# Optimization experiments

Hardware: AMD Instinct MI355X
Metric: run time of the kernel (lower is better)

The kernel has to match this reference:

```python
import jax, jax.numpy as jnp
import numpy as np

B, H, W, C, NH, WS, SS = 16, 112, 112, 384, 12, 7, 3
HD = C // NH          # head dim = 32
N = WS * WS           # tokens per window = 49
MLP_H = 4 * C         # 1536
NW = (H // WS) * (W // WS)  # windows per image = 256


def _rel_pos_index():
    coords = np.stack(np.meshgrid(np.arange(WS), np.arange(WS), indexing='ij')).reshape(2, -1)
    rel = (coords[:, :, None] - coords[:, None, :]).transpose(1, 2, 0)  # (N, N, 2)
    rel[..., 0] += WS - 1
    rel[..., 1] += WS - 1
    rel[..., 0] *= 2 * WS - 1
    return rel.sum(-1)  # (N, N) in [0, (2WS-1)^2)


def _attn_mask():
    img = np.zeros((H, W))
    cnt = 0
    slices = (slice(0, -WS), slice(-WS, -SS), slice(-SS, None))
    for hs in slices:
        for ws_ in slices:
            img[hs, ws_] = cnt
            cnt += 1
    mw = img.reshape(H // WS, WS, W // WS, WS).transpose(0, 2, 1, 3).reshape(-1, N)
    am = mw[:, None, :] - mw[:, :, None]
    return np.where(am != 0, -100.0, 0.0).astype(np.float32)  # (NW, N, N)


REL_IDX = jnp.asarray(_rel_pos_index().reshape(-1))  # (N*N,) int
MASK = jnp.asarray(_attn_mask())                      # (NW, N, N)


def _ln(x, g, b, eps=1e-5):
    m = jnp.mean(x, -1, keepdims=True)
    v = jnp.mean((x - m) ** 2, -1, keepdims=True)
    return (x - m) / jnp.sqrt(v + eps) * g + b


def setup_inputs() -> dict:
    key = jax.random.key(0)
    ks = jax.random.split(key, 16)
    s = 0.02
    return {
        'x': jax.random.normal(ks[0], (B, H * W, C), jnp.float32),
        'norm1_g': jnp.ones((C,), jnp.float32),
        'norm1_b': jnp.zeros((C,), jnp.float32),
        'qkv_w': jax.random.normal(ks[1], (C, 3 * C), jnp.float32) * s,
        'qkv_b': jnp.zeros((3 * C,), jnp.float32),
        'proj_w': jax.random.normal(ks[2], (C, C), jnp.float32) * s,
        'proj_b': jnp.zeros((C,), jnp.float32),
        'rpb_table': jax.random.normal(ks[3], ((2 * WS - 1) ** 2, NH), jnp.float32) * s,
        'norm2_g': jnp.ones((C,), jnp.float32),
        'norm2_b': jnp.zeros((C,), jnp.float32),
        'fc1_w': jax.random.normal(ks[4], (C, MLP_H), jnp.float32) * s,
        'fc1_b': jnp.zeros((MLP_H,), jnp.float32),
        'fc2_w': jax.random.normal(ks[5], (MLP_H, C), jnp.float32) * s,
        'fc2_b': jnp.zeros((C,), jnp.float32),
    }


def reference(x, norm1_g, norm1_b, qkv_w, qkv_b, proj_w, proj_b, rpb_table,
              norm2_g, norm2_b, fc1_w, fc1_b, fc2_w, fc2_b):
    shortcut = x
    h = _ln(x, norm1_g, norm1_b).reshape(B, H, W, C)
    # cyclic shift
    h = jnp.roll(h, (-SS, -SS), axis=(1, 2))
    # window partition -> (B*NW, N, C)
    wins = h.reshape(B, H // WS, WS, W // WS, WS, C).transpose(0, 1, 3, 2, 4, 5).reshape(-1, N, C)
    qkv = (wins @ qkv_w + qkv_b).reshape(-1, N, 3, NH, HD).transpose(2, 0, 3, 1, 4)
    q, k, v = qkv[0] * HD ** -0.5, qkv[1], qkv[2]  # (B*NW, NH, N, HD)
    attn = jnp.einsum('bhnd,bhmd->bhnm', q, k)
    bias = rpb_table[REL_IDX].reshape(N, N, NH).transpose(2, 0, 1)  # (NH, N, N)
    attn = attn + bias[None]
    attn = (attn.reshape(B, NW, NH, N, N) + MASK[None, :, None]).reshape(-1, NH, N, N)
    attn = jax.nn.softmax(attn, axis=-1)
    out = jnp.einsum('bhnm,bhmd->bhnd', attn, v).transpose(0, 2, 1, 3).reshape(-1, N, C)
    out = out @ proj_w + proj_b
    # window reverse
    out = out.reshape(B, H // WS, W // WS, WS, WS, C).transpose(0, 1, 3, 2, 4, 5).reshape(B, H, W, C)
    out = jnp.roll(out, (SS, SS), axis=(1, 2)).reshape(B, H * W, C)
    x = shortcut + out
    h2 = _ln(x, norm2_g, norm2_b)
    h2 = jax.nn.gelu(h2 @ fc1_w + fc1_b, approximate=False) @ fc2_w + fc2_b
    return x + h2
```

## Files before the change

### kernel.cpp

```cpp
#include <hip/hip_runtime.h>
#include <hip/hip_bf16.h>

typedef short bf16x8 __attribute__((ext_vector_type(8)));
typedef float f32x4 __attribute__((ext_vector_type(4)));
typedef float f32x16 __attribute__((ext_vector_type(16)));
typedef unsigned int u32x4 __attribute__((ext_vector_type(4)));

typedef __attribute__((address_space(1))) void gvoid;
typedef __attribute__((address_space(3))) void lvoid;

__device__ __forceinline__ short f2b(float f) {
  __hip_bfloat16 h = __float2bfloat16(f);
  return __builtin_bit_cast(short, h);
}

__device__ __forceinline__ f32x4 mfma16(bf16x8 a, bf16x8 b, f32x4 c) {
  return __builtin_amdgcn_mfma_f32_16x16x32_bf16(a, b, c, 0, 0, 0);
}

__device__ __forceinline__ f32x16 mfma32(bf16x8 a, bf16x8 b, f32x16 c) {
  return __builtin_amdgcn_mfma_f32_32x32x16_bf16(a, b, c, 0, 0, 0);
}

__device__ __forceinline__ unsigned cvtpk(float lo, float hi) {
  unsigned r;
  asm("v_cvt_pk_bf16_f32 %0, %1, %2" : "=v"(r) : "v"(lo), "v"(hi));
  return r;
}

__device__ __forceinline__ void gload16(const void* g, void* l) {
  __builtin_amdgcn_global_load_lds((const gvoid*)g, (lvoid*)l, 16, 0, 0);
}

__global__ __launch_bounds__(256) void convT_k(const float* __restrict__ src,
                                               short* __restrict__ dst, int K,
                                               int N, int scale_cols,
                                               float scale) {
  int idx = blockIdx.x * 256 + threadIdx.x;
  if (idx >= N * K) return;
  int n = idx / K, k = idx % K;
  float v = src[(size_t)k * N + n];
  if (n < scale_cols) v *= scale;
  dst[idx] = f2b(v);
}

__global__ __launch_bounds__(256) void scale_bias_k(const float* __restrict__ src,
                                                    float* __restrict__ dst,
                                                    int n, int scale_cols,
                                                    float scale) {
  int i = blockIdx.x * 256 + threadIdx.x;
  if (i >= n) return;
  dst[i] = src[i] * (i < scale_cols ? scale : 1.f);
}

__global__ __launch_bounds__(256) void biasmask_k(const float* __restrict__ rpb,
                                                  float* __restrict__ tbl) {
  int idx = blockIdx.x * 256 + threadIdx.x;
  int q = idx & 63, key = (idx >> 6) & 63;
  int hc = idx >> 12;
  int h = hc % 12, cls = hc / 12;
  float v;
  if (q >= 49 || key >= 49) {
    v = -1e4f;
  } else {
    int i1 = q / 7, j1 = q % 7, i2 = key / 7, j2 = key % 7;
    v = rpb[(size_t)((i1 - i2 + 6) * 13 + (j1 - j2 + 6)) * 12 + h];
    int clsh = cls >> 1, clsw = cls & 1;
    int rq = (clsh ? 1 + (i1 >= 4) : 0) * 3 + (clsw ? 1 + (j1 >= 4) : 0);
    int rk = (clsh ? 1 + (i2 >= 4) : 0) * 3 + (clsw ? 1 + (j2 >= 4) : 0);
    if (rq != rk) v -= 100.f;
  }
  tbl[idx] = v;
}

template <bool GATHER>
__device__ __forceinline__ void ln_body(const float* __restrict__ x,
                                        const float* __restrict__ gw,
                                        const float* __restrict__ bw,
                                        short* __restrict__ out) {
  const int lane = threadIdx.x & 63;
  const int t = (blockIdx.x << 2) + (threadIdx.x >> 6);
  size_t srow;
  if (GATHER) {
    int bb = t / 12544, rm2 = t % 12544;
    int wi = rm2 / 49, nn = rm2 % 49;
    int wh = wi >> 4, ww = wi & 15;
    int ii = nn / 7, jj = nn % 7;
    int rr = wh * 7 + ii + 3; if (rr >= 112) rr -= 112;
    int cc = ww * 7 + jj + 3; if (cc >= 112) cc -= 112;
    srow = ((size_t)bb * 12544 + rr * 112 + cc) * 384;
  } else {
    srow = (size_t)t * 384;
  }
  const float2* src = (const float2*)(x + srow);
  const float2* g2 = (const float2*)gw;
  const float2* b2 = (const float2*)bw;
  float2 u[3];
  float s = 0.f, ss = 0.f;
#pragma unroll
  for (int k = 0; k < 3; ++k) {
    u[k] = src[lane + (k << 6)];
    s += u[k].x + u[k].y;
    ss += u[k].x * u[k].x + u[k].y * u[k].y;
  }
#pragma unroll
  for (int m = 1; m < 64; m <<= 1) {
    s += __shfl_xor(s, m, 64);
    ss += __shfl_xor(ss, m, 64);
  }
  const float mean = s * (1.f / 384.f);
  const float var = ss * (1.f / 384.f) - mean * mean;
  const float rstd = rsqrtf(var + 1e-5f);
  unsigned* o = (unsigned*)(out + (size_t)t * 384);
#pragma unroll
  for (int k = 0; k < 3; ++k) {
    int c = lane + (k << 6);
    float2 gv = g2[c], bv = b2[c];
    unsigned lo = (unsigned short)f2b((u[k].x - mean) * rstd * gv.x + bv.x);
    unsigned hi = (unsigned short)f2b((u[k].y - mean) * rstd * gv.y + bv.y);
    o[c] = lo | (hi << 16);
  }
}

__global__ __launch_bounds__(256) void ln1_k(const float* __restrict__ x,
                                             const float* __restrict__ gw,
                                             const float* __restrict__ bw,
                                             short* __restrict__ out) {
  ln_body<true>(x, gw, bw, out);
}
__global__ __launch_bounds__(256) void ln2_k(const float* __restrict__ x,
                                             const float* __restrict__ gw,
                                             const float* __restrict__ bw,
                                             short* __restrict__ out) {
  ln_body<false>(x, gw, bw, out);
}

template <int EPI>
__device__ __forceinline__ void gemm_body(
    const short* __restrict__ A, int lda, const short* __restrict__ BT,
    int ldb, const float* __restrict__ bias, int K, short* __restrict__ outh,
    int ldo, float* __restrict__ outf, const float* __restrict__ resid) {
  __shared__ __align__(16) short As0[4096], Bs0[4096];
  __shared__ __align__(16) short As1[4096], Bs1[4096];
  const int tid = threadIdx.x;
  const int gx = gridDim.x;
  int lin = blockIdx.y * gx + blockIdx.x;
  const int cpx = (gx * gridDim.y) >> 3;
  lin = (lin & 7) * cpx + (lin >> 3);
  const int m0 = (lin / gx) << 7, n0 = (lin % gx) << 7;
  const int lane = tid & 63;
  const int wave = tid >> 6;
  const int wr = (wave >> 1) << 6, wc = (wave & 1) << 6;
  const int g = lane >> 4, q = lane & 15;
  const int loff = tid << 3;

  f32x4 acc[4][4];
#pragma unroll
  for (int i = 0; i < 4; ++i)
#pragma unroll
    for (int j = 0; j < 4; ++j) acc[i][j] = (f32x4){0.f, 0.f, 0.f, 0.f};

  const short* Ab = A + (size_t)(m0 + (tid >> 2)) * lda + ((tid & 3) << 3);
  const short* Ab2 = Ab + (size_t)64 * lda;
  const short* Bb = BT + (size_t)(n0 + (tid >> 2)) * ldb + ((tid & 3) << 3);
  const short* Bb2 = Bb + (size_t)64 * ldb;

#define STAGE(kt, dA, dB)                   \
  do {                                      \
    gload16(Ab + (kt), &dA[loff]);          \
    gload16(Ab2 + (kt), &dA[loff + 2048]);  \
    gload16(Bb + (kt), &dB[loff]);          \
    gload16(Bb2 + (kt), &dB[loff + 2048]);  \
  } while (0)

#define COMPUTE(SA, SB)                                               \
  do {                                                                \
    bf16x8 af[4], bfv[4];                                             \
    _Pragma("unroll") for (int mi = 0; mi < 4; ++mi)                  \
        af[mi] = *(const bf16x8*)&SA[(wr + mi * 16 + q) * 32 + g * 8];\
    _Pragma("unroll") for (int ni = 0; ni < 4; ++ni)                  \
        bfv[ni] = *(const bf16x8*)&SB[(wc + ni * 16 + q) * 32 + g * 8];\
    _Pragma("unroll") for (int mi = 0; mi < 4; ++mi)                  \
        _Pragma("unroll") for (int ni = 0; ni < 4; ++ni)              \
            acc[mi][ni] = mfma16(af[mi], bfv[ni], acc[mi][ni]);       \
  } while (0)

  const int nt = K >> 5;
  STAGE(0, As0, Bs0);
  __syncthreads();
  for (int t = 0; t < nt; t += 2) {
    STAGE((t + 1) << 5, As1, Bs1);
    COMPUTE(As0, Bs0);
    __syncthreads();
    if (t + 2 < nt) STAGE((t + 2) << 5, As0, Bs0);
    COMPUTE(As1, Bs1);
    __syncthreads();
  }
#undef STAGE
#undef COMPUTE

  float bv[4];
#pragma unroll
  for (int ni = 0; ni < 4; ++ni)
    bv[ni] = bias ? bias[n0 + wc + ni * 16 + q] : 0.f;

#pragma unroll
  for (int mi = 0; mi < 4; ++mi) {
#pragma unroll
    for (int r = 0; r < 4; ++r) {
      const int grow = m0 + wr + mi * 16 + g * 4 + r;
      size_t orow;
      if constexpr (EPI == 2) {
        int bb = grow / 12544, rm2 = grow % 12544;
        int wi = rm2 / 49, nn = rm2 % 49;
        int wh = wi >> 4, ww = wi & 15;
        int ii = nn / 7, jj = nn % 7;
        int rr = wh * 7 + ii + 3; if (rr >= 112) rr -= 112;
        int cc = ww * 7 + jj + 3; if (cc >= 112) cc -= 112;
        orow = ((size_t)bb * 12544 + rr * 112 + cc) * 384;
      } else {
        orow = (size_t)grow * (size_t)ldo;
      }
#pragma unroll
      for (int ni = 0; ni < 4; ++ni) {
        const int gcol = n0 + wc + ni * 16 + q;
        float v = acc[mi][ni][r] + bv[ni];
        if constexpr (EPI == 0) {
          outh[orow + gcol] = f2b(v);
        } else if constexpr (EPI == 1) {
          v = 0.5f * v * (1.f + erff(v * 0.70710678118f));
          outh[orow + gcol] = f2b(v);
        } else if constexpr (EPI == 2) {
          outf[orow + gcol] = resid[orow + gcol] + v;
        } else {
          outf[orow + gcol] += v;
        }
      }
    }
  }
}

#define GEMM_WRAP(NAME, EPI)                                                   \
  __global__ __launch_bounds__(256) void NAME(                                 \
      const short* __restrict__ A, int lda, const short* __restrict__ BT,      \
      int ldb, const float* __restrict__ bias, int K,                          \
      short* __restrict__ outh, int ldo, float* __restrict__ outf,             \
      const float* __restrict__ resid) {                                       \
    gemm_body<EPI>(A, lda, BT, ldb, bias, K, outh, ldo, outf, resid);          \
  }
GEMM_WRAP(gemm_qkv_k, 0)
GEMM_WRAP(gemm_fc1_k, 1)
GEMM_WRAP(gemm_proj_k, 2)
GEMM_WRAP(gemm_fc2_k, 3)

__global__ __launch_bounds__(256) void attn_k(const short* __restrict__ qkv,
                                              const float* __restrict__ tbl,
                                              short* __restrict__ out) {
  const int lane = threadIdx.x & 63;
  const int task = blockIdx.x * 4 + (threadIdx.x >> 6);
  const int win = task / 12;
  const int h = task - win * 12;
  const int wh = (win >> 4) & 15, ww = win & 15;
  const int cls = ((wh == 15) ? 2 : 0) + ((ww == 15) ? 1 : 0);
  const int l31 = lane & 31, h5 = lane >> 5;
  const size_t tokbase = (size_t)win * 49;
  const short* base = qkv + tokbase * 1152 + h * 32;
  const bf16x8 zero8 = {0, 0, 0, 0, 0, 0, 0, 0};

  bf16x8 kf[2][2];
#pragma unroll
  for (int mi = 0; mi < 2; ++mi) {
    int row = l31 + 32 * mi;
#pragma unroll
    for (int s = 0; s < 2; ++s)
      kf[mi][s] = (row < 49)
                      ? *(const bf16x8*)(base + (size_t)row * 1152 + 384 +
                                         16 * s + 8 * h5)
                      : zero8;
  }
  bf16x8 vf[4];
#pragma unroll
  for (int kt = 0; kt < 4; ++kt) {
#pragma unroll
    for (int e = 0; e < 8; ++e) {
      int key = 16 * kt + 8 * h5 + e;
      vf[kt][e] = (key < 49) ? base[(size_t)key * 1152 + 768 + l31] : (short)0;
    }
  }

  const float* tb = tbl + ((size_t)(cls * 12 + h) << 12);

#pragma unroll
  for (int ni = 0; ni < 2; ++ni) {
    bf16x8 qf[2];
    int qrow = l31 + 32 * ni;
#pragma unroll
    for (int s = 0; s < 2; ++s)
      qf[s] = (qrow < 49)
                  ? *(const bf16x8*)(base + (size_t)qrow * 1152 + 16 * s +
                                     8 * h5)
                  : zero8;
    f32x16 st[2];
#pragma unroll
    for (int mi = 0; mi < 2; ++mi) {
      st[mi] = mfma32(kf[mi][0], qf[0], (f32x16)(0.f));
      st[mi] = mfma32(kf[mi][1], qf[1], st[mi]);
    }
#pragma unroll
    for (int mi = 0; mi < 2; ++mi)
#pragma unroll
      for (int r = 0; r < 16; ++r) {
        int koff = (r & 3) + 8 * (r >> 2) + 4 * h5;
        st[mi][r] += tb[(size_t)(32 * mi + koff) * 64 + 32 * ni + l31];
      }
    float mx = st[0][0];
#pragma unroll
    for (int r = 1; r < 16; ++r) mx = fmaxf(mx, st[0][r]);
#pragma unroll
    for (int r = 0; r < 16; ++r) mx = fmaxf(mx, st[1][r]);
    mx = fmaxf(mx, __shfl_xor(mx, 32, 64));
    float sm = 0.f;
#pragma unroll
    for (int mi = 0; mi < 2; ++mi)
#pragma unroll
      for (int r = 0; r < 16; ++r) {
        float e = __expf(st[mi][r] - mx);
        st[mi][r] = e;
        sm += e;
      }
    sm += __shfl_xor(sm, 32, 64);
    const float rinv = 1.f / sm;
#pragma unroll
    for (int mi = 0; mi < 2; ++mi)
#pragma unroll
      for (int r = 0; r < 16; ++r) st[mi][r] *= rinv;

    f32x16 acc = (f32x16)(0.f);
#pragma unroll
    for (int kt = 0; kt < 4; ++kt) {
      const int mi = kt >> 1, b8 = (kt & 1) * 8;
      unsigned q0l = cvtpk(st[mi][b8 + 0], st[mi][b8 + 1]);
      unsigned q0h = cvtpk(st[mi][b8 + 2], st[mi][b8 + 3]);
      unsigned q1l = cvtpk(st[mi][b8 + 4], st[mi][b8 + 5]);
      unsigned q1h = cvtpk(st[mi][b8 + 6], st[mi][b8 + 7]);
      unsigned sl = h5 ? q0l : q1l, sh = h5 ? q0h : q1h;
      unsigned kl = h5 ? q1l : q0l, kh = h5 ? q1h : q0h;
      unsigned rl = (unsigned)__shfl_xor((int)sl, 32, 64);
      unsigned rh = (unsigned)__shfl_xor((int)sh, 32, 64);
      u32x4 fr;
      fr[0] = h5 ? rl : kl;
      fr[1] = h5 ? rh : kh;
      fr[2] = h5 ? kl : rl;
      fr[3] = h5 ? kh : rh;
      acc = mfma32(__builtin_bit_cast(bf16x8, fr), vf[kt], acc);
    }
#pragma unroll
    for (int r = 0; r < 16; ++r) {
      int query = 32 * ni + (r & 3) + 8 * (r >> 2) + 4 * h5;
      if (ni == 0 || query < 49)
        out[(tokbase + query) * 384 + h * 32 + l31] = f2b(acc[r]);
    }
  }
}

extern "C" void kernel_launch(void* const* d_in, const int* in_sizes, int n_in,
                              void* d_out, int out_size, void* d_ws,
                              size_t ws_size, hipStream_t stream) {
  const float* x = (const float*)d_in[0];
  const float* n1g = (const float*)d_in[1];
  const float* n1b = (const float*)d_in[2];
  const float* qkvw = (const float*)d_in[3];
  const float* qkvb = (const float*)d_in[4];
  const float* projw = (const float*)d_in[5];
  const float* projb = (const float*)d_in[6];
  const float* rpb = (const float*)d_in[7];
  const float* n2g = (const float*)d_in[8];
  const float* n2b = (const float*)d_in[9];
  const float* fc1w = (const float*)d_in[10];
  const float* fc1b = (const float*)d_in[11];
  const float* fc2w = (const float*)d_in[12];
  const float* fc2b = (const float*)d_in[13];
  float* out = (float*)d_out;

  char* ws = (char*)d_ws;
  short* w_qkvT = (short*)(ws + 0);
  short* w_projT = (short*)(ws + 884736);
  short* w_fc1T = (short*)(ws + 1179648);
  short* w_fc2T = (short*)(ws + 2359296);
  float* w_qb = (float*)(ws + 3538944);
  float* tbl = (float*)(ws + 3543552);
  const size_t o_qkv = 4329984;
  short* qkvbuf = (short*)(ws + o_qkv);
  const size_t o_hwin = o_qkv + 462422016ull;
  short* hwin = (short*)(ws + o_hwin);
  const size_t o_fc1 = o_hwin + 154140672ull;

  int NC;
  size_t fc1_off = o_fc1;
  if (ws_size >= o_fc1 + 616562688ull) NC = 1;
  else if (ws_size >= o_fc1 + 308281344ull) NC = 2;
  else if (ws_size >= o_fc1 + 154140672ull) NC = 4;
  else { NC = 4; fc1_off = o_hwin; }
  short* fc1c = (short*)(ws + fc1_off);
  short* h2 = qkvbuf;

  const float qscale = 0.17677669529663687f;

  convT_k<<<(442368 + 255) / 256, 256, 0, stream>>>(qkvw, w_qkvT, 384, 1152, 384, qscale);
  convT_k<<<(147456 + 255) / 256, 256, 0, stream>>>(projw, w_projT, 384, 384, 0, 1.f);
  convT_k<<<(589824 + 255) / 256, 256, 0, stream>>>(fc1w, w_fc1T, 384, 1536, 0, 1.f);
  convT_k<<<(589824 + 255) / 256, 256, 0, stream>>>(fc2w, w_fc2T, 1536, 384, 0, 1.f);
  scale_bias_k<<<5, 256, 0, stream>>>(qkvb, w_qb, 1152, 384, qscale);
  biasmask_k<<<768, 256, 0, stream>>>(rpb, tbl);

  ln1_k<<<50176, 256, 0, stream>>>(x, n1g, n1b, hwin);
  gemm_qkv_k<<<dim3(9, 1568), 256, 0, stream>>>(hwin, 384, w_qkvT, 384, w_qb,
                                                384, qkvbuf, 1152, nullptr,
                                                nullptr);
  attn_k<<<12288, 256, 0, stream>>>(qkvbuf, tbl, hwin);
  gemm_proj_k<<<dim3(3, 1568), 256, 0, stream>>>(hwin, 384, w_projT, 384,
                                                 projb, 384, nullptr, 384, out,
                                                 x);
  ln2_k<<<50176, 256, 0, stream>>>(out, n2g, n2b, h2);
  const int CK = 1536 / NC;
  for (int c = 0; c < NC; ++c) {
    gemm_fc1_k<<<dim3(CK >> 7, 1568), 256, 0, stream>>>(
        h2, 384, w_fc1T + (size_t)c * CK * 384, 384, fc1b + c * CK, 384, fc1c,
        CK, nullptr, nullptr);
    gemm_fc2_k<<<dim3(3, 1568), 256, 0, stream>>>(
        fc1c, CK, w_fc2T + c * CK, 1536, (c == 0) ? fc2b : nullptr, CK,
        nullptr, 384, out, nullptr);
  }
}
```

Baseline: 2.159 ms.

## Triple-buffer GEMM LDS pipeline with partial vmcnt waits and MFMA priority

Converts the GEMM main loop from double-buffered LDS staging with full __syncthreads to a three-stage ring. Two tiles are kept in flight, and s_waitcnt vmcnt(4) plus a raw barrier wait only for the oldest tile. It also raises wave priority around the MFMA block and adds a launch-bounds occupancy hint of 3 blocks per CU. The aim is to hide global-load latency behind compute. In exchange, LDS use grows from 32KB to 48KB per block, which can limit occupancy, and the hand-written waitcnt logic depends on the exact count of outstanding loads.

```diff
diff --git a/kernel.cpp b/kernel.cpp
--- a/kernel.cpp
+++ b/kernel.cpp
@@ -140,8 +140,9 @@
     const short* __restrict__ A, int lda, const short* __restrict__ BT,
     int ldb, const float* __restrict__ bias, int K, short* __restrict__ outh,
     int ldo, float* __restrict__ outf, const float* __restrict__ resid) {
-  __shared__ __align__(16) short As0[4096], Bs0[4096];
-  __shared__ __align__(16) short As1[4096], Bs1[4096];
+  __shared__ __align__(16) short A0[4096], B0[4096];
+  __shared__ __align__(16) short A1[4096], B1[4096];
+  __shared__ __align__(16) short A2[4096], B2[4096];
   const int tid = threadIdx.x;
   const int gx = gridDim.x;
   int lin = blockIdx.y * gx + blockIdx.x;
@@ -180,24 +181,43 @@
         af[mi] = *(const bf16x8*)&SA[(wr + mi * 16 + q) * 32 + g * 8];\
     _Pragma("unroll") for (int ni = 0; ni < 4; ++ni)                  \
         bfv[ni] = *(const bf16x8*)&SB[(wc + ni * 16 + q) * 32 + g * 8];\
+    __builtin_amdgcn_s_setprio(1);                                    \
     _Pragma("unroll") for (int mi = 0; mi < 4; ++mi)                  \
         _Pragma("unroll") for (int ni = 0; ni < 4; ++ni)              \
             acc[mi][ni] = mfma16(af[mi], bfv[ni], acc[mi][ni]);       \
+    __builtin_amdgcn_s_setprio(0);                                    \
   } while (0)
 
+#define VM4 asm volatile("s_waitcnt vmcnt(4)" ::: "memory")
+#define VM0 asm volatile("s_waitcnt vmcnt(0)" ::: "memory")
+#define BAR __builtin_amdgcn_s_barrier()
+
   const int nt = K >> 5;
-  STAGE(0, As0, Bs0);
-  __syncthreads();
-  for (int t = 0; t < nt; t += 2) {
-    STAGE((t + 1) << 5, As1, Bs1);
-    COMPUTE(As0, Bs0);
-    __syncthreads();
-    if (t + 2 < nt) STAGE((t + 2) << 5, As0, Bs0);
-    COMPUTE(As1, Bs1);
-    __syncthreads();
+  STAGE(0, A0, B0);
+  STAGE(32, A1, B1);
+  VM4;
+  BAR;
+  for (int t = 0; t < nt; t += 3) {
+    if (t + 2 < nt) STAGE((t + 2) << 5, A2, B2);
+    COMPUTE(A0, B0);
+    if (t + 2 < nt) VM4; else VM0;
+    BAR;
+    if (t + 1 >= nt) break;
+    if (t + 3 < nt) STAGE((t + 3) << 5, A0, B0);
+    COMPUTE(A1, B1);
+    if (t + 3 < nt) VM4; else VM0;
+    BAR;
+    if (t + 2 >= nt) break;
+    if (t + 4 < nt) STAGE((t + 4) << 5, A1, B1);
+    COMPUTE(A2, B2);
+    if (t + 4 < nt) VM4; else VM0;
+    BAR;
   }
 #undef STAGE
 #undef COMPUTE
+#undef VM4
+#undef VM0
+#undef BAR
 
   float bv[4];
 #pragma unroll
@@ -241,7 +261,7 @@
 }
 
 #define GEMM_WRAP(NAME, EPI)                                                   \
-  __global__ __launch_bounds__(256) void NAME(                                 \
+  __global__ __launch_bounds__(256, 3) void NAME(                              \
       const short* __restrict__ A, int lda, const short* __restrict__ BT,      \
       int ldb, const float* __restrict__ bias, int K,                          \
       short* __restrict__ outh, int ldo, float* __restrict__ outf,             \
```

Measured after the change: 6.819 ms. 216% more time.

## Stream GEMM B operand via registers and triple-buffer swizzled A tiles

Applied to the files above, without the earlier changes.

The GEMM main loop is restructured. The B (weight) fragments are now loaded straight from global memory into registers, one k-step ahead, instead of being staged through LDS. A tiles are triple-buffered in LDS with an XOR swizzle that is meant to avoid bank conflicts. Explicit vmcnt waits and raw s_barrier replace __syncthreads, so the global loads for the next two k-steps can overlap the MFMA work. The aim is to cut LDS traffic and barrier stalls, at the cost of less coalesced B loads that rely on L2 hits, and a hand-unrolled loop whose tail is only correct for particular values of K/32.

```diff
diff --git a/kernel.cpp b/kernel.cpp
--- a/kernel.cpp
+++ b/kernel.cpp
@@ -140,8 +140,9 @@
     const short* __restrict__ A, int lda, const short* __restrict__ BT,
     int ldb, const float* __restrict__ bias, int K, short* __restrict__ outh,
     int ldo, float* __restrict__ outf, const float* __restrict__ resid) {
-  __shared__ __align__(16) short As0[4096], Bs0[4096];
-  __shared__ __align__(16) short As1[4096], Bs1[4096];
+  __shared__ __align__(16) short A0s[4096];
+  __shared__ __align__(16) short A1s[4096];
+  __shared__ __align__(16) short A2s[4096];
   const int tid = threadIdx.x;
   const int gx = gridDim.x;
   int lin = blockIdx.y * gx + blockIdx.x;
@@ -153,6 +154,8 @@
   const int wr = (wave >> 1) << 6, wc = (wave & 1) << 6;
   const int g = lane >> 4, q = lane & 15;
   const int loff = tid << 3;
+  const int cswz = (tid & 3) ^ ((tid >> 3) & 3);
+  const int cpos = (g ^ ((q >> 1) & 3)) << 3;
 
   f32x4 acc[4][4];
 #pragma unroll
@@ -160,44 +163,88 @@
 #pragma unroll
     for (int j = 0; j < 4; ++j) acc[i][j] = (f32x4){0.f, 0.f, 0.f, 0.f};
 
-  const short* Ab = A + (size_t)(m0 + (tid >> 2)) * lda + ((tid & 3) << 3);
+  const short* Ab = A + (size_t)(m0 + (tid >> 2)) * lda + cswz * 8;
   const short* Ab2 = Ab + (size_t)64 * lda;
-  const short* Bb = BT + (size_t)(n0 + (tid >> 2)) * ldb + ((tid & 3) << 3);
-  const short* Bb2 = Bb + (size_t)64 * ldb;
-
-#define STAGE(kt, dA, dB)                   \
-  do {                                      \
-    gload16(Ab + (kt), &dA[loff]);          \
-    gload16(Ab2 + (kt), &dA[loff + 2048]);  \
-    gload16(Bb + (kt), &dB[loff]);          \
-    gload16(Bb2 + (kt), &dB[loff + 2048]);  \
-  } while (0)
-
-#define COMPUTE(SA, SB)                                               \
-  do {                                                                \
-    bf16x8 af[4], bfv[4];                                             \
-    _Pragma("unroll") for (int mi = 0; mi < 4; ++mi)                  \
-        af[mi] = *(const bf16x8*)&SA[(wr + mi * 16 + q) * 32 + g * 8];\
-    _Pragma("unroll") for (int ni = 0; ni < 4; ++ni)                  \
-        bfv[ni] = *(const bf16x8*)&SB[(wc + ni * 16 + q) * 32 + g * 8];\
-    _Pragma("unroll") for (int mi = 0; mi < 4; ++mi)                  \
-        _Pragma("unroll") for (int ni = 0; ni < 4; ++ni)              \
-            acc[mi][ni] = mfma16(af[mi], bfv[ni], acc[mi][ni]);       \
-  } while (0)
-
+  const short* Bq = BT + (size_t)(n0 + wc + q) * ldb + g * 8;
+  const size_t bstep = (size_t)16 * ldb;
+
+#define STAGE_A(kt, DA)                    \
+  do {                                     \
+    gload16(Ab + (kt), &DA[loff]);         \
+    gload16(Ab2 + (kt), &DA[loff + 2048]); \
+  } while (0)
+
+#define BLOAD(BF, kt)                                                     \
+  do {                                                                    \
+    _Pragma("unroll") for (int ni = 0; ni < 4; ++ni)                      \
+        BF[ni] = *(const bf16x8*)(Bq + (size_t)ni * bstep + (kt));        \
+  } while (0)
+
+#define COMPUTE(SA, BF)                                                   \
+  do {                                                                    \
+    bf16x8 af[4];                                                         \
+    _Pragma("unroll") for (int mi = 0; mi < 4; ++mi)                      \
+        af[mi] = *(const bf16x8*)&SA[(wr + mi * 16 + q) * 32 + cpos];     \
+    _Pragma("unroll") for (int mi = 0; mi < 4; ++mi)                      \
+        _Pragma("unroll") for (int ni = 0; ni < 4; ++ni)                  \
+            acc[mi][ni] = mfma16(af[mi], BF[ni], acc[mi][ni]);            \
+  } while (0)
+
+#define VMW2                                          \
+  do {                                                \
+    asm volatile("s_waitcnt vmcnt(2)" ::: "memory");  \
+    __builtin_amdgcn_sched_barrier(0);                \
+  } while (0)
+#define VMW0                                          \
+  do {                                                \
+    asm volatile("s_waitcnt vmcnt(0)" ::: "memory");  \
+    __builtin_amdgcn_sched_barrier(0);                \
+  } while (0)
+#define BAR __builtin_amdgcn_s_barrier()
+
+  bf16x8 bfA[4], bfB[4];
   const int nt = K >> 5;
-  STAGE(0, As0, Bs0);
-  __syncthreads();
-  for (int t = 0; t < nt; t += 2) {
-    STAGE((t + 1) << 5, As1, Bs1);
-    COMPUTE(As0, Bs0);
-    __syncthreads();
-    if (t + 2 < nt) STAGE((t + 2) << 5, As0, Bs0);
-    COMPUTE(As1, Bs1);
-    __syncthreads();
-  }
-#undef STAGE
+
+  BLOAD(bfA, 0);
+  STAGE_A(0, A0s);
+  STAGE_A(32, A1s);
+  VMW2;
+  BAR;
+
+#define PH(BFC, BFN, SCUR, SNXT, tt)     \
+  do {                                   \
+    BLOAD(BFN, ((tt) + 1) << 5);         \
+    STAGE_A(((tt) + 2) << 5, SNXT);      \
+    COMPUTE(SCUR, BFC);                  \
+    VMW2;                                \
+    BAR;                                 \
+  } while (0)
+
+  int t = 0;
+  for (; t + 6 < nt; t += 6) {
+    PH(bfA, bfB, A0s, A2s, t + 0);
+    PH(bfB, bfA, A1s, A0s, t + 1);
+    PH(bfA, bfB, A2s, A1s, t + 2);
+    PH(bfB, bfA, A0s, A2s, t + 3);
+    PH(bfA, bfB, A1s, A0s, t + 4);
+    PH(bfB, bfA, A2s, A1s, t + 5);
+  }
+  PH(bfA, bfB, A0s, A2s, t + 0);
+  PH(bfB, bfA, A1s, A0s, t + 1);
+  PH(bfA, bfB, A2s, A1s, t + 2);
+  PH(bfB, bfA, A0s, A2s, t + 3);
+  BLOAD(bfB, (t + 5) << 5);
+  COMPUTE(A1s, bfA);
+  VMW0;
+  BAR;
+  COMPUTE(A2s, bfB);
+#undef STAGE_A
+#undef BLOAD
 #undef COMPUTE
+#undef VMW2
+#undef VMW0
+#undef BAR
+#undef PH
 
   float bv[4];
 #pragma unroll
```

New measurement: 2.709 ms. +25.5%, slower.

## Double GEMM K-tile to 64 and XOR-swizzle LDS layout

Applied to the files above, without the earlier changes.

The GEMM body now stages 64-wide K tiles instead of 32, which halves the number of barriers and pipeline iterations per block. Global loads write into LDS using an XOR-swizzled column order, and the MFMA fragment reads apply the matching swizzle to avoid LDS bank conflicts. LDS use per block doubles to 64 KB, which may lower occupancy. K must now be a multiple of 128 for the two-buffer loop to stay correct.

```diff
diff --git a/kernel.cpp b/kernel.cpp
--- a/kernel.cpp
+++ b/kernel.cpp
@@ -140,8 +140,8 @@
     const short* __restrict__ A, int lda, const short* __restrict__ BT,
     int ldb, const float* __restrict__ bias, int K, short* __restrict__ outh,
     int ldo, float* __restrict__ outf, const float* __restrict__ resid) {
-  __shared__ __align__(16) short As0[4096], Bs0[4096];
-  __shared__ __align__(16) short As1[4096], Bs1[4096];
+  __shared__ __align__(16) short A0s[8192], B0s[8192];
+  __shared__ __align__(16) short A1s[8192], B1s[8192];
   const int tid = threadIdx.x;
   const int gx = gridDim.x;
   int lin = blockIdx.y * gx + blockIdx.x;
@@ -152,7 +152,11 @@
   const int wave = tid >> 6;
   const int wr = (wave >> 1) << 6, wc = (wave & 1) << 6;
   const int g = lane >> 4, q = lane & 15;
-  const int loff = tid << 3;
+  const int q7 = q & 7;
+  const int rd0 = ((g) ^ q7) << 3;
+  const int rd1 = ((4 + g) ^ q7) << 3;
+  const int cswz = ((tid & 7) ^ ((tid >> 3) & 7)) << 3;
+  const int ldst = tid << 3;
 
   f32x4 acc[4][4];
 #pragma unroll
@@ -160,40 +164,41 @@
 #pragma unroll
     for (int j = 0; j < 4; ++j) acc[i][j] = (f32x4){0.f, 0.f, 0.f, 0.f};
 
-  const short* Ab = A + (size_t)(m0 + (tid >> 2)) * lda + ((tid & 3) << 3);
-  const short* Ab2 = Ab + (size_t)64 * lda;
-  const short* Bb = BT + (size_t)(n0 + (tid >> 2)) * ldb + ((tid & 3) << 3);
-  const short* Bb2 = Bb + (size_t)64 * ldb;
-
-#define STAGE(kt, dA, dB)                   \
-  do {                                      \
-    gload16(Ab + (kt), &dA[loff]);          \
-    gload16(Ab2 + (kt), &dA[loff + 2048]);  \
-    gload16(Bb + (kt), &dB[loff]);          \
-    gload16(Bb2 + (kt), &dB[loff + 2048]);  \
+  const short* Abase = A + (size_t)(m0 + (tid >> 3)) * lda + cswz;
+  const short* Bbase = BT + (size_t)(n0 + (tid >> 3)) * ldb + cswz;
+
+#define STAGE(kt, DA, DB)                                                     \
+  do {                                                                        \
+    _Pragma("unroll") for (int p = 0; p < 4; ++p) {                           \
+      gload16(Abase + (size_t)(32 * p) * lda + (kt), &DA[2048 * p + ldst]);   \
+      gload16(Bbase + (size_t)(32 * p) * ldb + (kt), &DB[2048 * p + ldst]);   \
+    }                                                                         \
   } while (0)
 
-#define COMPUTE(SA, SB)                                               \
-  do {                                                                \
-    bf16x8 af[4], bfv[4];                                             \
-    _Pragma("unroll") for (int mi = 0; mi < 4; ++mi)                  \
-        af[mi] = *(const bf16x8*)&SA[(wr + mi * 16 + q) * 32 + g * 8];\
-    _Pragma("unroll") for (int ni = 0; ni < 4; ++ni)                  \
-        bfv[ni] = *(const bf16x8*)&SB[(wc + ni * 16 + q) * 32 + g * 8];\
-    _Pragma("unroll") for (int mi = 0; mi < 4; ++mi)                  \
-        _Pragma("unroll") for (int ni = 0; ni < 4; ++ni)              \
-            acc[mi][ni] = mfma16(af[mi], bfv[ni], acc[mi][ni]);       \
+#define COMPUTE(SA, SB)                                                       \
+  do {                                                                        \
+    _Pragma("unroll") for (int kk = 0; kk < 2; ++kk) {                        \
+      const int rdo = kk ? rd1 : rd0;                                         \
+      bf16x8 af[4], bfv[4];                                                   \
+      _Pragma("unroll") for (int mi = 0; mi < 4; ++mi)                        \
+          af[mi] = *(const bf16x8*)&SA[(wr + mi * 16 + q) * 64 + rdo];        \
+      _Pragma("unroll") for (int ni = 0; ni < 4; ++ni)                        \
+          bfv[ni] = *(const bf16x8*)&SB[(wc + ni * 16 + q) * 64 + rdo];       \
+      _Pragma("unroll") for (int mi = 0; mi < 4; ++mi)                        \
+          _Pragma("unroll") for (int ni = 0; ni < 4; ++ni)                    \
+              acc[mi][ni] = mfma16(af[mi], bfv[ni], acc[mi][ni]);             \
+    }                                                                         \
   } while (0)
 
-  const int nt = K >> 5;
-  STAGE(0, As0, Bs0);
+  const int nt = K >> 6;
+  STAGE(0, A0s, B0s);
   __syncthreads();
   for (int t = 0; t < nt; t += 2) {
-    STAGE((t + 1) << 5, As1, Bs1);
-    COMPUTE(As0, Bs0);
+    STAGE((t + 1) << 6, A1s, B1s);
+    COMPUTE(A0s, B0s);
     __syncthreads();
-    if (t + 2 < nt) STAGE((t + 2) << 5, As0, Bs0);
-    COMPUTE(As1, Bs1);
+    if (t + 2 < nt) STAGE((t + 2) << 6, A0s, B0s);
+    COMPUTE(A1s, B1s);
     __syncthreads();
   }
 #undef STAGE
```

Result: no change. 2.128 ms (-1.4%).
